# Optimization experiments

Measured on AMD Instinct MI355X. Metric: run time of the kernel, lower is better.

## Reference

```python
import jax, jax.numpy as jnp
import numpy as np

W = 5; WW = 25; STEP = 8; DF = 128; NH = 8; DH = 16; EPS = 1e-5


def sinusoid_pe(ww, d):
    pos = np.arange(ww)[:, None].astype(np.float32)
    div = np.exp(np.arange(0, d, 2).astype(np.float32) * (-np.log(10000.0) / d))
    pe = np.zeros((ww, d), np.float32)
    pe[:, 0::2] = np.sin(pos * div)
    pe[:, 1::2] = np.cos(pos * div)
    return jnp.asarray(pe)


def ln(x, s, b):
    m = x.mean(-1, keepdims=True)
    v = ((x - m) ** 2).mean(-1, keepdims=True)
    return (x - m) / jnp.sqrt(v + EPS) * s + b


def attn_layer(x, src, wq, wk, wv, wm, m1w, m1b, m2w, m2b, n1s, n1b, n2s, n2b):
    N, T, D = x.shape
    q = (x @ wq).reshape(N, T, NH, DH)
    k = (src @ wk).reshape(N, T, NH, DH)
    v = (src @ wv).reshape(N, T, NH, DH)
    a = jax.nn.softmax(jnp.einsum('nqhd,nkhd->nhqk', q, k) * (DH ** -0.5), axis=-1)
    msg = jnp.einsum('nhqk,nkhd->nqhd', a, v).reshape(N, T, D) @ wm
    msg = ln(msg, n1s, n1b)
    h = jnp.concatenate([x, msg], axis=-1)
    h = jax.nn.relu(h @ m1w + m1b) @ m2w + m2b
    return x + ln(h, n2s, n2b)


def local_transformer(x0, x1, P):
    names = ['self', 'cross', 'self', 'cross']
    for i, nm in enumerate(names):
        p = tuple(a[i] for a in P)
        if nm == 'self':
            x0 = attn_layer(x0, x0, *p)
            x1 = attn_layer(x1, x1, *p)
        else:
            x0 = attn_layer(x0, x1, *p)
            x1 = attn_layer(x1, x0, *p)
    return x0, x1


def unfold_window(fm):
    # F.unfold(kernel=5, stride=4, pad=2) then 'B (C MM) L -> B L MM C'
    B, C, H, Wd = fm.shape
    pat = jax.lax.conv_general_dilated_patches(fm, (W, W), (4, 4), [(W // 2, W // 2)] * 2)
    Ho, Wo = pat.shape[2], pat.shape[3]
    pat = pat.reshape(B, C, WW, Ho * Wo)  # channel-major ordering matches torch unfold
    return pat.transpose(0, 3, 2, 1)  # [B, L, WW, C]


def forward(mdesc0, mdesc1, fine0, fine1, conv_w, conv_b, proj_w, proj_b,
            merge_w, merge_b, reg1_w, reg1_b, reg2_w, reg2_b, reg_w, reg_b,
            lt_wq, lt_wk, lt_wv, lt_wm, lt_m1w, lt_m1b, lt_m2w, lt_m2b,
            lt_n1s, lt_n1b, lt_n2s, lt_n2b):
    B, L, Dc = mdesc0.shape
    Wc = int(np.sqrt(L))
    # dual-softmax confidence matrix
    sim = jnp.einsum('bld,bmd->blm', mdesc0 / Dc, mdesc1 / Dc) / 0.1
    cm = jax.nn.softmax(sim, axis=1) * jax.nn.softmax(sim, axis=2)
    # mutual nearest-neighbor filter (static-shape: keep all B*L rows + mask)
    mut = (cm == cm.max(axis=2, keepdims=True)) & (cm == cm.max(axis=1, keepdims=True))
    cf = cm * mut
    mask = cf.max(axis=2) > 0  # [B, L]
    j = jnp.argmax(cf, axis=2)  # [B, L]
    # 1x1 conv to fine dim
    f0 = jnp.einsum('bchw,oc->bohw', fine0, conv_w[:, :, 0, 0]) + conv_b[None, :, None, None]
    f1 = jnp.einsum('bchw,oc->bohw', fine1, conv_w[:, :, 0, 0]) + conv_b[None, :, None, None]
    u0 = unfold_window(f0)
    u1 = unfold_window(f1)  # [B, L, WW, DF]
    N = B * L
    b_all = jnp.repeat(jnp.arange(B), L)
    idx1 = b_all * L + j.reshape(-1)
    local0 = u0.reshape(N, WW, DF)
    local1 = u1.reshape(N, WW, DF)[idx1]
    c0 = mdesc0.reshape(N, Dc)
    c1 = mdesc1.reshape(N, Dc)[idx1]
    local = jnp.concatenate([local0, local1], axis=0)  # [2N, WW, DF]
    center = jnp.concatenate([c0, c1], axis=0) @ proj_w + proj_b  # [2N, DF]
    center = jnp.broadcast_to(center[:, None, :], (2 * N, WW, DF))
    ld = jnp.concatenate([local, center], axis=-1) @ merge_w + merge_b
    ld = ld + sinusoid_pe(WW, DF)[None]
    d0, d1 = ld[:N], ld[N:]
    P = (lt_wq, lt_wk, lt_wv, lt_wm, lt_m1w, lt_m1b, lt_m2w, lt_m2b, lt_n1s, lt_n1b, lt_n2s, lt_n2b)
    fd0, fd1 = local_transformer(d0, d1, P)
    c = WW // 2
    cen = jnp.broadcast_to(fd0[:, c:c + 1, :], (N, WW, DF))
    feat = jnp.concatenate([cen, fd1], axis=-1)  # [N, WW, 2*DF]
    feat = feat @ reg1_w + reg1_b  # [N, WW, DF]
    feat = feat.reshape(N, WW * DF)  # [N, 3200]
    feat = feat @ reg2_w + reg2_b  # dropout is identity at eval
    coords = feat @ reg_w + reg_b  # [N, 2]
    xj = (j % Wc) * STEP
    yj = (j // Wc) * STEP
    base = jnp.stack([xj, yj], axis=-1).reshape(N, 2).astype(coords.dtype)
    return (base + coords) * mask.reshape(N, 1).astype(coords.dtype)


def setup_inputs():
    key = jax.random.key(0)
    ks = jax.random.split(key, 24)
    B, L, Dc = 2, 2304, 256
    Hf = 192
    nl = 4

    def rn(k, shape, fan):
        return jax.random.normal(k, shape, jnp.float32) * (fan ** -0.5)

    return {
        'mdesc0': jax.random.normal(ks[0], (B, L, Dc), jnp.float32),
        'mdesc1': jax.random.normal(ks[1], (B, L, Dc), jnp.float32),
        'fine0': jax.random.normal(ks[2], (B, Dc, Hf, Hf), jnp.float32),
        'fine1': jax.random.normal(ks[3], (B, Dc, Hf, Hf), jnp.float32),
        'conv_w': rn(ks[4], (DF, Dc, 1, 1), Dc),
        'conv_b': jnp.zeros((DF,), jnp.float32),
        'proj_w': rn(ks[5], (Dc, DF), Dc),
        'proj_b': jnp.zeros((DF,), jnp.float32),
        'merge_w': rn(ks[6], (2 * DF, DF), 2 * DF),
        'merge_b': jnp.zeros((DF,), jnp.float32),
        'reg1_w': rn(ks[7], (2 * DF, DF), 2 * DF),
        'reg1_b': jnp.zeros((DF,), jnp.float32),
        'reg2_w': rn(ks[8], (WW * DF, DF), WW * DF),
        'reg2_b': jnp.zeros((DF,), jnp.float32),
        'reg_w': rn(ks[9], (DF, 2), DF),
        'reg_b': jnp.zeros((2,), jnp.float32),
        'lt_wq': rn(ks[10], (nl, DF, DF), DF),
        'lt_wk': rn(ks[11], (nl, DF, DF), DF),
        'lt_wv': rn(ks[12], (nl, DF, DF), DF),
        'lt_wm': rn(ks[13], (nl, DF, DF), DF),
        'lt_m1w': rn(ks[14], (nl, 2 * DF, 2 * DF), 2 * DF),
        'lt_m1b': jnp.zeros((nl, 2 * DF), jnp.float32),
        'lt_m2w': rn(ks[15], (nl, 2 * DF, DF), 2 * DF),
        'lt_m2b': jnp.zeros((nl, DF), jnp.float32),
        'lt_n1s': jnp.ones((nl, DF), jnp.float32),
        'lt_n1b': jnp.zeros((nl, DF), jnp.float32),
        'lt_n2s': jnp.ones((nl, DF), jnp.float32),
        'lt_n2b': jnp.zeros((nl, DF), jnp.float32),
    }


def reference(mdesc0, mdesc1, fine0, fine1, conv_w, conv_b, proj_w, proj_b,
              merge_w, merge_b, reg1_w, reg1_b, reg2_w, reg2_b, reg_w, reg_b,
              lt_wq, lt_wk, lt_wv, lt_wm, lt_m1w, lt_m1b, lt_m2w, lt_m2b,
              lt_n1s, lt_n1b, lt_n2s, lt_n2b):
    return forward(mdesc0, mdesc1, fine0, fine1, conv_w, conv_b, proj_w, proj_b,
                   merge_w, merge_b, reg1_w, reg1_b, reg2_w, reg2_b, reg_w, reg_b,
                   lt_wq, lt_wk, lt_wv, lt_wm, lt_m1w, lt_m1b, lt_m2w, lt_m2b,
                   lt_n1s, lt_n1b, lt_n2s, lt_n2b)
```

## Files before the change

kernel.cpp:

```cpp
#include <hip/hip_runtime.h>
#include <stdint.h>
#include <type_traits>

#define DEVFN static __device__ __forceinline__

typedef __attribute__((ext_vector_type(8))) short bf16x8v;
typedef __attribute__((ext_vector_type(4))) float f32x4v;
typedef __attribute__((ext_vector_type(2))) _Float16 h2;

DEVFN float b2f(short s) {
  union { unsigned u; float f; } c; c.u = ((unsigned)(unsigned short)s) << 16; return c.f;
}
DEVFN short f2b(float f) {
  union { float f; unsigned u; } c; c.f = f;
  unsigned r = c.u + 0x7fffu + ((c.u >> 16) & 1u);
  return (short)(r >> 16);
}
DEVFN short f2h(float f) {
  union { _Float16 h; short s; } c; c.h = (_Float16)f; return c.s;
}
DEVFN void gl_lds16(const void* g, void* l) {
  __builtin_amdgcn_global_load_lds((const __attribute__((address_space(1))) void*)g,
                                   (__attribute__((address_space(3))) void*)l, 16, 0, 0);
}
DEVFN double exp_small(double x) {
  return 1.0 + x * (1.0 + x * (0.5 + x * ((1.0 / 6.0) + x * (1.0 / 24.0))));
}


__global__ void prep_all(const float* __restrict__ conv_w, const float* __restrict__ proj_w,
                         const float* __restrict__ merge_w, const float* __restrict__ reg1_w,
                         const float* __restrict__ reg2_w, const float* __restrict__ wq,
                         const float* __restrict__ wk, const float* __restrict__ wv,
                         const float* __restrict__ wm, const float* __restrict__ m1w,
                         const float* __restrict__ m2w,
                         short* __restrict__ convT, short* __restrict__ projT,
                         short* __restrict__ mergeAT, short* __restrict__ mergeBT,
                         short* __restrict__ reg1T, short* __restrict__ reg2T,
                         short* __restrict__ wqkvT, short* __restrict__ wmT,
                         short* __restrict__ m1T, short* __restrict__ m2T,
                         float* __restrict__ pe, short* __restrict__ zp) {
  const int L0 = 32768, L1 = 32768, L2 = 16384, L3 = 16384, L4 = 32768, L5 = 409600;
  const int L6 = 196608, L7 = 65536, L8 = 262144, L9 = 131072, L10 = 3200, L11 = 128;
  const int TOT = L0+L1+L2+L3+L4+L5+L6+L7+L8+L9+L10+L11;
  for (int gi = blockIdx.x * blockDim.x + threadIdx.x; gi < TOT; gi += gridDim.x * blockDim.x) {
    int i = gi;
    if (i < L0) { convT[i] = f2b(conv_w[i]); continue; } i -= L0;
    if (i < L1) { int n = i >> 8, k = i & 255; projT[i] = f2b(proj_w[k * 128 + n]); continue; } i -= L1;
    if (i < L2) { int n = i >> 7, k = i & 127; mergeAT[i] = f2b(merge_w[k * 128 + n]); continue; } i -= L2;
    if (i < L3) { int n = i >> 7, k = i & 127; mergeBT[i] = f2b(merge_w[(128 + k) * 128 + n]); continue; } i -= L3;
    if (i < L4) { int n = i >> 8, k = i & 255; reg1T[i] = f2b(reg1_w[k * 128 + n]); continue; } i -= L4;
    if (i < L5) { int n = i / 3200, k = i - n * 3200; reg2T[i] = f2b(reg2_w[k * 128 + n]); continue; } i -= L5;
    if (i < L6) {
      int l = i / 49152; int r = i - l * 49152; int w = r / 16384; int r2 = r - w * 16384;
      int n = r2 >> 7, k = r2 & 127;
      const float* s = (w == 0) ? wq : (w == 1) ? wk : wv;
      wqkvT[i] = f2b(s[l * 16384 + k * 128 + n]); continue;
    } i -= L6;
    if (i < L7) { int l = i >> 14; int r = i & 16383; int n = r >> 7, k = r & 127;
      wmT[i] = f2b(wm[l * 16384 + k * 128 + n]); continue; } i -= L7;
    if (i < L8) { int l = i >> 16; int r = i & 65535; int n = r >> 8, k = r & 255;
      m1T[i] = f2b(m1w[l * 65536 + k * 256 + n]); continue; } i -= L8;
    if (i < L9) { int l = i >> 15; int r = i & 32767; int n = r >> 8, k = r & 255;
      m2T[i] = f2b(m2w[l * 32768 + k * 128 + n]); continue; } i -= L9;
    if (i < L10) {
      int t = i >> 7, d = i & 127; int i2 = d >> 1;
      float div = expf(((float)(2 * i2)) * (-logf(10000.f) / 128.f));
      float ang = (float)t * div;
      pe[i] = (d & 1) ? cosf(ang) : sinf(ang); continue;
    } i -= L10;
    zp[i] = 0;
  }
}


__global__ __launch_bounds__(256) void sim_gemm(const float* __restrict__ A,
                                                const float* __restrict__ Bm,
                                                float* __restrict__ S) {
  int b = blockIdx.z;
  A += (size_t)b * 2304 * 256; Bm += (size_t)b * 2304 * 256; S += (size_t)b * 2304 * 2304;
  __shared__ float As[96][33], Bs[96][33];
  int tid = threadIdx.x;
  int tx = tid & 15, ty = tid >> 4;
  int rb = blockIdx.x * 96, cb = blockIdx.y * 96;
  float acc[6][6] = {};
  for (int k0 = 0; k0 < 256; k0 += 32) {
    #pragma unroll
    for (int s = 0; s < 3; ++s) {
      int slot = s * 256 + tid;
      int r = slot >> 3, cq = slot & 7;
      float4 va = *(const float4*)&A[(size_t)(rb + r) * 256 + k0 + 4 * cq];
      float4 vb = *(const float4*)&Bm[(size_t)(cb + r) * 256 + k0 + 4 * cq];
      As[r][4 * cq] = va.x; As[r][4 * cq + 1] = va.y; As[r][4 * cq + 2] = va.z; As[r][4 * cq + 3] = va.w;
      Bs[r][4 * cq] = vb.x; Bs[r][4 * cq + 1] = vb.y; Bs[r][4 * cq + 2] = vb.z; Bs[r][4 * cq + 3] = vb.w;
    }
    __syncthreads();
    #pragma unroll 4
    for (int k = 0; k < 32; ++k) {
      float av[6], bv[6];
      #pragma unroll
      for (int i = 0; i < 6; ++i) av[i] = As[ty + 16 * i][k];
      #pragma unroll
      for (int j = 0; j < 6; ++j) bv[j] = Bs[tx + 16 * j][k];
      #pragma unroll
      for (int i = 0; i < 6; ++i)
        #pragma unroll
        for (int j = 0; j < 6; ++j) acc[i][j] += av[i] * bv[j];
    }
    __syncthreads();
  }
  #pragma unroll
  for (int i = 0; i < 6; ++i)
    #pragma unroll
    for (int j = 0; j < 6; ++j) {
      float t = acc[i][j] * (1.0f / 65536.0f);
      S[(size_t)(rb + ty + 16 * i) * 2304 + cb + tx + 16 * j] = t / 0.1f;
    }
}

__global__ __launch_bounds__(256) void row_lse(const float* __restrict__ S, double* __restrict__ lnR) {
  int row = blockIdx.x;
  const float* Sp = S + (size_t)row * 2304;
  double a = 0;
  for (int m = threadIdx.x; m < 2304; m += 256) a += exp_small((double)Sp[m]);
  __shared__ double red[256];
  red[threadIdx.x] = a; __syncthreads();
  for (int s = 128; s > 0; s >>= 1) { if (threadIdx.x < (unsigned)s) red[threadIdx.x] += red[threadIdx.x + s]; __syncthreads(); }
  if (!threadIdx.x) lnR[row] = log(red[0]);
}

__global__ __launch_bounds__(256) void col_part(const float* __restrict__ S,
                                                const double* __restrict__ lnR,
                                                double* __restrict__ psum,
                                                double* __restrict__ pkey,
                                                int* __restrict__ pidx) {
  int bb = blockIdx.z;
  int c0 = blockIdx.x * 64;
  int rc = blockIdx.y;
  int col = c0 + (threadIdx.x & 63);
  int g = threadIdx.x >> 6;
  const float* Sp = S + (size_t)bb * 2304 * 2304;
  const double* lr = lnR + bb * 2304;
  double a = 0, best = -1e300; int bi = 1 << 30;
  int l0 = rc * 192;
  for (int t = g; t < 192; t += 4) {
    int l = l0 + t;
    double sv = (double)Sp[(size_t)l * 2304 + col];
    a += exp_small(sv);
    double k = 2.0 * sv - lr[l];
    if (k > best || (k == best && l < bi)) { best = k; bi = l; }
  }
  __shared__ double s_sum[256]; __shared__ double s_key[256]; __shared__ int s_idx[256];
  s_sum[threadIdx.x] = a; s_key[threadIdx.x] = best; s_idx[threadIdx.x] = bi;
  __syncthreads();
  if (g == 0) {
    double ts = a; double tk = best; int ti = bi;
    #pragma unroll
    for (int gg = 1; gg < 4; ++gg) {
      int o = threadIdx.x + gg * 64;
      ts += s_sum[o];
      if (s_key[o] > tk || (s_key[o] == tk && s_idx[o] < ti)) { tk = s_key[o]; ti = s_idx[o]; }
    }
    size_t off = ((size_t)bb * 12 + rc) * 2304 + col;
    psum[off] = ts; pkey[off] = tk; pidx[off] = ti;
  }
}

__global__ void col_reduce(const double* __restrict__ psum, const double* __restrict__ pkey,
                           const int* __restrict__ pidx, double* __restrict__ lnC,
                           int* __restrict__ CB) {
  int i = blockIdx.x * blockDim.x + threadIdx.x;
  if (i >= 4608) return;
  int bb = i / 2304, col = i - bb * 2304;
  double s = 0; double bk = -1e300; int bi = 1 << 30;
  for (int rc = 0; rc < 12; ++rc) {
    size_t off = ((size_t)bb * 12 + rc) * 2304 + col;
    s += psum[off];
    double k = pkey[off]; int ix = pidx[off];
    if (k > bk || (k == bk && ix < bi)) { bk = k; bi = ix; }
  }
  lnC[i] = log(s);
  CB[i] = bi;
}

__global__ __launch_bounds__(256) void row_argmax(const float* __restrict__ S,
                                                  const double* __restrict__ lnC,
                                                  int* __restrict__ J) {
  int row = blockIdx.x; int bb = row / 2304;
  const float* Sp = S + (size_t)row * 2304;
  const double* lc = lnC + bb * 2304;
  double best = -1e300; int bi = 1 << 30;
  for (int m = threadIdx.x; m < 2304; m += 256) {
    double k = 2.0 * (double)Sp[m] - lc[m];
    if (k > best || (k == best && m < bi)) { best = k; bi = m; }
  }
  __shared__ double bvs[256]; __shared__ int bis[256];
  bvs[threadIdx.x] = best; bis[threadIdx.x] = bi; __syncthreads();
  for (int s = 128; s > 0; s >>= 1) {
    if (threadIdx.x < (unsigned)s) {
      double ov = bvs[threadIdx.x + s]; int oi = bis[threadIdx.x + s];
      if (ov > bvs[threadIdx.x] || (ov == bvs[threadIdx.x] && oi < bis[threadIdx.x])) { bvs[threadIdx.x] = ov; bis[threadIdx.x] = oi; }
    }
    __syncthreads();
  }
  if (!threadIdx.x) J[row] = bis[0];
}


__global__ __launch_bounds__(256) void transpose_fine(const float* __restrict__ src, short* __restrict__ dst) {
  __shared__ float t[64][65];
  int bb = blockIdx.z, p0 = blockIdx.x * 64, c0 = blockIdx.y * 64;
  for (int i = threadIdx.x; i < 1024; i += 256) {
    int cl = i >> 4, pl = (i & 15) * 4;
    float4 v = *(const float4*)&src[((size_t)(bb * 256 + c0 + cl)) * 36864 + p0 + pl];
    t[cl][pl] = v.x; t[cl][pl + 1] = v.y; t[cl][pl + 2] = v.z; t[cl][pl + 3] = v.w;
  }
  __syncthreads();
  for (int i = threadIdx.x; i < 1024; i += 256) {
    int pl = i >> 4, cg = (i & 15) * 4;
    unsigned w0 = (unsigned short)f2b(t[cg][pl]) | ((unsigned)(unsigned short)f2b(t[cg + 1][pl]) << 16);
    unsigned w1 = (unsigned short)f2b(t[cg + 2][pl]) | ((unsigned)(unsigned short)f2b(t[cg + 3][pl]) << 16);
    int2 v; v.x = (int)w0; v.y = (int)w1;
    *(int2*)&dst[((size_t)(bb * 36864 + p0 + pl)) * 256 + c0 + cg] = v;
  }
}

__global__ void cgather(const float* __restrict__ md0, const float* __restrict__ md1,
                        const int* __restrict__ J, short* __restrict__ cbuf) {
  int total = 9216 * 256;
  for (int i = blockIdx.x * blockDim.x + threadIdx.x; i < total; i += gridDim.x * blockDim.x) {
    int w = i >> 8, c = i & 255;
    const float* src;
    if (w < 4608) src = md0 + (size_t)w * 256;
    else {
      int n = w - 4608; int bb = n / 2304;
      src = md1 + (size_t)(bb * 2304 + J[n]) * 256;
    }
    cbuf[i] = f2b(src[c]);
  }
}

__global__ void build_tab(const int* __restrict__ J, const short* __restrict__ f0c,
                          const short* __restrict__ f1c, const short* __restrict__ zp,
                          unsigned long long* __restrict__ tab) {
  int total = 230400;
  for (int i = blockIdx.x * blockDim.x + threadIdx.x; i < total; i += gridDim.x * blockDim.x) {
    int w = i / 25, t = i - w * 25;
    int bb, cell; const short* fc;
    if (w < 4608) { bb = w / 2304; cell = w - bb * 2304; fc = f0c; }
    else { int n = w - 4608; bb = n / 2304; cell = J[n]; fc = f1c; }
    int cy = cell / 48, cx = cell - cy * 48;
    int y = cy * 4 - 2 + t / 5, x = cx * 4 - 2 + t % 5;
    const short* p = (y >= 0 && y < 192 && x >= 0 && x < 192)
                   ? fc + (size_t)((bb * 192 + y) * 192 + x) * 128 : zp;
    tab[i] = (unsigned long long)(uintptr_t)p;
  }
}


constexpr int AM_LIN = 0, AM_DUAL = 1, AM_TAB = 2, AM_CEN = 3;
constexpr int EP_BIAS = 0, EP_BF32 = 1, EP_RELU = 2, EP_LN = 3, EP_LNRES = 4, EP_MERGE = 5, EP_PART = 6, EP_F16 = 7;

template<int AMODE, int EPI>
__global__ __launch_bounds__(256)
void gemm_bf16(const short* __restrict__ A1, const short* __restrict__ A2,
               const unsigned long long* __restrict__ tab,
               const short* __restrict__ Wt, int M, int Kd, int kstr, int K1,
               const float* __restrict__ bias, int bstride,
               const float* __restrict__ lns, const float* __restrict__ lnb,
               const short* __restrict__ resid,
               const float* __restrict__ ccp, const float* __restrict__ pep,
               short* __restrict__ outb, float* __restrict__ outf, int ldc,
               long wstride, long ostride) {
  __shared__ __align__(16) short As[128 * 64];
  __shared__ __align__(16) short Bs[128 * 64];
  __shared__ float rsum[2][128], rsq[2][128];
  int tid = threadIdx.x, lane = tid & 63, wid = tid >> 6;
  int wr = wid >> 1, wc = wid & 1;
  int nwg = gridDim.x;
  int orig = blockIdx.x;
  int qd = nwg >> 3, rm = nwg & 7;
  int xcd = orig & 7, offx = orig >> 3;
  int bx = (xcd < rm ? xcd * (qd + 1) : rm * (qd + 1) + (xcd - rm) * qd) + offx;
  int rb = bx * 128;
  int by = blockIdx.y;
  int koff = blockIdx.z * Kd;
  const short* Wsel = Wt + (size_t)by * wstride;
  const float* bsel = bias ? bias + (size_t)by * bstride : nullptr;
  short* osel_b = outb ? outb + (size_t)by * ostride : nullptr;
  float* osel_f = outf ? outf + (size_t)by * ostride : nullptr;

  f32x4v acc[4][4];
  #pragma unroll
  for (int i = 0; i < 4; ++i)
    #pragma unroll
    for (int j = 0; j < 4; ++j) acc[i][j] = (f32x4v){0.f, 0.f, 0.f, 0.f};

  for (int k0 = 0; k0 < Kd; k0 += 64) {
    #pragma unroll
    for (int q = 0; q < 4; ++q) {
      int i = (wid * 4 + q) * 64 + lane;
      int r = i >> 3, pch = i & 7;
      int c = pch ^ (r & 7);
      const short* src;
      if (AMODE == AM_LIN) {
        src = A1 + (size_t)(rb + r) * kstr + koff + k0 + c * 8;
      } else if (AMODE == AM_DUAL) {
        if (k0 < K1) src = A1 + (size_t)(rb + r) * K1 + k0 + c * 8;
        else         src = A2 + (size_t)(rb + r) * (Kd - K1) + (k0 - K1) + c * 8;
      } else if (AMODE == AM_CEN) {
        int rg = rb + r;
        if (k0 < K1) src = A1 + (size_t)((rg / 25) * 25 + 12) * K1 + k0 + c * 8;
        else         src = A2 + (size_t)rg * (Kd - K1) + (k0 - K1) + c * 8;
      } else {
        src = (const short*)(uintptr_t)tab[rb + r] + k0 + c * 8;
      }
      gl_lds16(src, &As[(size_t)i * 8]);
    }
    #pragma unroll
    for (int q = 0; q < 4; ++q) {
      int i = (wid * 4 + q) * 64 + lane;
      int r = i >> 3, pch = i & 7;
      int c = pch ^ (r & 7);
      gl_lds16(Wsel + (size_t)r * kstr + koff + k0 + c * 8, &Bs[(size_t)i * 8]);
    }
    __syncthreads();
    #pragma unroll
    for (int kk = 0; kk < 2; ++kk) {
      bf16x8v af[4], bfr[4];
      #pragma unroll
      for (int mi = 0; mi < 4; ++mi) {
        int r = wr * 64 + mi * 16 + (lane & 15);
        int c = kk * 4 + (lane >> 4);
        int pch = c ^ (r & 7);
        af[mi] = *(const bf16x8v*)&As[r * 64 + pch * 8];
      }
      #pragma unroll
      for (int ni = 0; ni < 4; ++ni) {
        int r = wc * 64 + ni * 16 + (lane & 15);
        int c = kk * 4 + (lane >> 4);
        int pch = c ^ (r & 7);
        bfr[ni] = *(const bf16x8v*)&Bs[r * 64 + pch * 8];
      }
      #pragma unroll
      for (int mi = 0; mi < 4; ++mi)
        #pragma unroll
        for (int ni = 0; ni < 4; ++ni)
          acc[mi][ni] = __builtin_amdgcn_mfma_f32_16x16x32_bf16(af[mi], bfr[ni], acc[mi][ni], 0, 0, 0);
    }
    __syncthreads();
  }

  int colloc[4];
  #pragma unroll
  for (int ni = 0; ni < 4; ++ni) colloc[ni] = wc * 64 + ni * 16 + (lane & 15);
  float bv[4];
  #pragma unroll
  for (int ni = 0; ni < 4; ++ni)
    bv[ni] = (EPI == EP_MERGE || EPI == EP_PART) ? 0.f : (bsel ? bsel[colloc[ni]] : 0.f);

  #pragma unroll
  for (int mi = 0; mi < 4; ++mi)
    #pragma unroll
    for (int ni = 0; ni < 4; ++ni)
      #pragma unroll
      for (int q = 0; q < 4; ++q) {
        float v = acc[mi][ni][q] + bv[ni];
        if (EPI == EP_RELU) v = fmaxf(v, 0.f);
        acc[mi][ni][q] = v;
      }

  if (EPI == EP_LN || EPI == EP_LNRES) {
    #pragma unroll
    for (int mi = 0; mi < 4; ++mi)
      #pragma unroll
      for (int q = 0; q < 4; ++q) {
        float s = 0.f, ss = 0.f;
        #pragma unroll
        for (int ni = 0; ni < 4; ++ni) { float v = acc[mi][ni][q]; s += v; ss += v * v; }
        s += __shfl_xor(s, 1, 64); ss += __shfl_xor(ss, 1, 64);
        s += __shfl_xor(s, 2, 64); ss += __shfl_xor(ss, 2, 64);
        s += __shfl_xor(s, 4, 64); ss += __shfl_xor(ss, 4, 64);
        s += __shfl_xor(s, 8, 64); ss += __shfl_xor(ss, 8, 64);
        int rl = wr * 64 + mi * 16 + (lane >> 4) * 4 + q;
        if ((lane & 15) == 0) { rsum[wc][rl] = s; rsq[wc][rl] = ss; }
      }
    __syncthreads();
  }

  #pragma unroll
  for (int mi = 0; mi < 4; ++mi)
    #pragma unroll
    for (int q = 0; q < 4; ++q) {
      int rl = wr * 64 + mi * 16 + (lane >> 4) * 4 + q;
      long rg = rb + rl;
      float mean = 0.f, rstd = 0.f;
      if (EPI == EP_LN || EPI == EP_LNRES) {
        float s = rsum[0][rl] + rsum[1][rl];
        float ss = rsq[0][rl] + rsq[1][rl];
        mean = s * (1.f / 128.f);
        float var = ss * (1.f / 128.f) - mean * mean;
        rstd = 1.f / sqrtf(var + 1e-5f);
      }
      int wv_ = 0, tv_ = 0;
      if (EPI == EP_MERGE) { wv_ = (int)(rg / 25); tv_ = (int)(rg - (long)wv_ * 25); }
      #pragma unroll
      for (int ni = 0; ni < 4; ++ni) {
        int cg = colloc[ni];
        float v = acc[mi][ni][q];
        if (EPI == EP_MERGE) v += ccp[(size_t)wv_ * 128 + cg] + pep[tv_ * 128 + cg];
        if (EPI == EP_LN || EPI == EP_LNRES) {
          v = (v - mean) * rstd * lns[cg] + lnb[cg];
          if (EPI == EP_LNRES) v += b2f(resid[(size_t)rg * 128 + cg]);
        }
        if (EPI == EP_BF32) osel_f[(size_t)rg * ldc + cg] = v;
        else if (EPI == EP_PART) osel_f[((size_t)blockIdx.z * M + rg) * ldc + cg] = v;
        else if (EPI == EP_F16) osel_b[(size_t)rg * ldc + cg] = f2h(v);
        else osel_b[(size_t)rg * ldc + cg] = f2b(v);
      }
    }
}

__global__ void reduce_part(const float* __restrict__ part, const float* __restrict__ bias,
                            short* __restrict__ out) {
  int i = blockIdx.x * blockDim.x + threadIdx.x;
  if (i >= 4608 * 128) return;
  int c = i & 127;
  float s = bias[c];
  #pragma unroll
  for (int z = 0; z < 5; ++z) s += part[(size_t)z * 4608 * 128 + i];
  out[i] = f2b(s);
}


template<bool CROSS>
__global__ __launch_bounds__(256)
void qkv_fused(const short* __restrict__ xq, const short* __restrict__ xkv,
               const short* __restrict__ wqkv, short* __restrict__ out, long ostride) {
  __shared__ __align__(16) short As[128 * 128];
  __shared__ __align__(16) short Bs[128 * 64];
  int tid = threadIdx.x, lane = tid & 63, wid = tid >> 6;
  int wr = wid >> 1, wc = wid & 1;
  int nwg = gridDim.x;
  int orig = blockIdx.x;
  int qd = nwg >> 3, rm = nwg & 7;
  int xcd = orig & 7, offx = orig >> 3;
  int bx = (xcd < rm ? xcd * (qd + 1) : rm * (qd + 1) + (xcd - rm) * qd) + offx;
  int rb = bx * 128;

  auto stageA = [&](const short* src) {
    #pragma unroll
    for (int q = 0; q < 8; ++q) {
      int i = (wid * 8 + q) * 64 + lane;
      int r = i >> 4, pch = i & 15;
      int c = pch ^ (r & 7);
      gl_lds16(src + (size_t)(rb + r) * 128 + c * 8, &As[(size_t)i * 8]);
    }
  };
  stageA(xq);

  #pragma unroll
  for (int w = 0; w < 3; ++w) {
    if (CROSS && w == 1) stageA(xkv);
    f32x4v acc[4][4];
    #pragma unroll
    for (int i = 0; i < 4; ++i)
      #pragma unroll
      for (int j = 0; j < 4; ++j) acc[i][j] = (f32x4v){0.f, 0.f, 0.f, 0.f};
    const short* Wsel = wqkv + (size_t)w * 16384;

    #pragma unroll
    for (int kt = 0; kt < 2; ++kt) {
      int k0 = kt * 64;
      #pragma unroll
      for (int q = 0; q < 4; ++q) {
        int i = (wid * 4 + q) * 64 + lane;
        int r = i >> 3, pch = i & 7;
        int c = pch ^ (r & 7);
        gl_lds16(Wsel + (size_t)r * 128 + k0 + c * 8, &Bs[(size_t)i * 8]);
      }
      __syncthreads();
      #pragma unroll
      for (int kk = 0; kk < 2; ++kk) {
        bf16x8v af[4], bfr[4];
        #pragma unroll
        for (int mi = 0; mi < 4; ++mi) {
          int r = wr * 64 + mi * 16 + (lane & 15);
          int cg = kt * 8 + kk * 4 + (lane >> 4);
          int pch = cg ^ (r & 7);
          af[mi] = *(const bf16x8v*)&As[r * 128 + pch * 8];
        }
        #pragma unroll
        for (int ni = 0; ni < 4; ++ni) {
          int r = wc * 64 + ni * 16 + (lane & 15);
          int c = kk * 4 + (lane >> 4);
          int pch = c ^ (r & 7);
          bfr[ni] = *(const bf16x8v*)&Bs[r * 64 + pch * 8];
        }
        #pragma unroll
        for (int mi = 0; mi < 4; ++mi)
          #pragma unroll
          for (int ni = 0; ni < 4; ++ni)
            acc[mi][ni] = __builtin_amdgcn_mfma_f32_16x16x32_bf16(af[mi], bfr[ni], acc[mi][ni], 0, 0, 0);
      }
      __syncthreads();
    }
    short* ow = out + (size_t)w * ostride;
    #pragma unroll
    for (int mi = 0; mi < 4; ++mi)
      #pragma unroll
      for (int q = 0; q < 4; ++q) {
        int rl = wr * 64 + mi * 16 + (lane >> 4) * 4 + q;
        long rg = rb + rl;
        #pragma unroll
        for (int ni = 0; ni < 4; ++ni) {
          int cg = wc * 64 + ni * 16 + (lane & 15);
          ow[(size_t)rg * 128 + cg] = f2h(acc[mi][ni][q]);
        }
      }
  }
}


__global__ __launch_bounds__(256)
void mlp2_fused(const short* __restrict__ x, const short* __restrict__ attnout,
                const short* __restrict__ wmT,
                const short* __restrict__ m1wT, const short* __restrict__ m2wT,
                const float* __restrict__ n1s, const float* __restrict__ n1b,
                const float* __restrict__ b1, const float* __restrict__ b2,
                const float* __restrict__ lns, const float* __restrict__ lnb,
                short* __restrict__ out) {
  __shared__ __align__(16) short AsHs[64 * 128];
  __shared__ __align__(16) short Bs[128 * 128];
  __shared__ __align__(16) short Ms[64 * 128];
  short* As = AsHs;
  short* Hs = AsHs;
  float* rsum = (float*)AsHs;
  float* rsq  = (float*)AsHs + 128;
  int tid = threadIdx.x, lane = tid & 63, wid = tid >> 6;
  int wr = wid >> 1, wc = wid & 1;
  int nwg = gridDim.x;
  int orig = blockIdx.x;
  int qd = nwg >> 3, rm = nwg & 7;
  int xcd = orig & 7, offx = orig >> 3;
  int bx = (xcd < rm ? xcd * (qd + 1) : rm * (qd + 1) + (xcd - rm) * qd) + offx;
  int rb = bx * 64;

  int colloc[4];
  #pragma unroll
  for (int ni = 0; ni < 4; ++ni) colloc[ni] = wc * 64 + ni * 16 + (lane & 15);

  auto stageA = [&](const short* src) {
    #pragma unroll
    for (int q = 0; q < 4; ++q) {
      int i = (wid * 4 + q) * 64 + lane;
      int r = i >> 4, pch = i & 15;
      int c = pch ^ (r & 7);
      gl_lds16(src + (size_t)(rb + r) * 128 + c * 8, &As[(size_t)i * 8]);
    }
  };
  auto stageB = [&](const short* src, int kstr) {
    #pragma unroll
    for (int q = 0; q < 8; ++q) {
      int i = (wid * 8 + q) * 64 + lane;
      int r = i >> 4, pch = i & 15;
      int c = pch ^ (r & 7);
      gl_lds16(src + (size_t)r * kstr + c * 8, &Bs[(size_t)i * 8]);
    }
  };
  auto mfmaAB = [&](const short* Atile, f32x4v (*acc)[4]) {
    #pragma unroll
    for (int kk = 0; kk < 4; ++kk) {
      bf16x8v af[2], bfr[4];
      #pragma unroll
      for (int mi = 0; mi < 2; ++mi) {
        int r = wr * 32 + mi * 16 + (lane & 15);
        int c = kk * 4 + (lane >> 4);
        int pch = c ^ (r & 7);
        af[mi] = *(const bf16x8v*)&Atile[r * 128 + pch * 8];
      }
      #pragma unroll
      for (int ni = 0; ni < 4; ++ni) {
        int r = wc * 64 + ni * 16 + (lane & 15);
        int c = kk * 4 + (lane >> 4);
        int pch = c ^ (r & 7);
        bfr[ni] = *(const bf16x8v*)&Bs[r * 128 + pch * 8];
      }
      #pragma unroll
      for (int mi = 0; mi < 2; ++mi)
        #pragma unroll
        for (int ni = 0; ni < 4; ++ni)
          acc[mi][ni] = __builtin_amdgcn_mfma_f32_16x16x32_bf16(af[mi], bfr[ni], acc[mi][ni], 0, 0, 0);
    }
  };

  {
    f32x4v acc0[2][4];
    #pragma unroll
    for (int i = 0; i < 2; ++i)
      #pragma unroll
      for (int j = 0; j < 4; ++j) acc0[i][j] = (f32x4v){0.f, 0.f, 0.f, 0.f};
    stageA(attnout);
    stageB(wmT, 128);
    __syncthreads();
    mfmaAB(As, acc0);
    __syncthreads();
    #pragma unroll
    for (int mi = 0; mi < 2; ++mi)
      #pragma unroll
      for (int q = 0; q < 4; ++q) {
        float s = 0.f, ss = 0.f;
        #pragma unroll
        for (int ni = 0; ni < 4; ++ni) { float v = acc0[mi][ni][q]; s += v; ss += v * v; }
        s += __shfl_xor(s, 1, 64); ss += __shfl_xor(ss, 1, 64);
        s += __shfl_xor(s, 2, 64); ss += __shfl_xor(ss, 2, 64);
        s += __shfl_xor(s, 4, 64); ss += __shfl_xor(ss, 4, 64);
        s += __shfl_xor(s, 8, 64); ss += __shfl_xor(ss, 8, 64);
        int rl = wr * 32 + mi * 16 + (lane >> 4) * 4 + q;
        if ((lane & 15) == 0) { rsum[wc * 64 + rl] = s; rsq[wc * 64 + rl] = ss; }
      }
    __syncthreads();
    #pragma unroll
    for (int mi = 0; mi < 2; ++mi)
      #pragma unroll
      for (int q = 0; q < 4; ++q) {
        int rl = wr * 32 + mi * 16 + (lane >> 4) * 4 + q;
        float s = rsum[rl] + rsum[64 + rl];
        float ss = rsq[rl] + rsq[64 + rl];
        float mean = s * (1.f / 128.f);
        float var = ss * (1.f / 128.f) - mean * mean;
        float rstd = 1.f / sqrtf(var + 1e-5f);
        #pragma unroll
        for (int ni = 0; ni < 4; ++ni) {
          int cg = colloc[ni];
          float v = (acc0[mi][ni][q] - mean) * rstd * n1s[cg] + n1b[cg];
          int c = cg >> 3, pch = c ^ (rl & 7);
          Ms[rl * 128 + pch * 8 + (cg & 7)] = f2b(v);
        }
      }
    __syncthreads();
  }

  f32x4v acc2[2][4];
  #pragma unroll
  for (int i = 0; i < 2; ++i)
    #pragma unroll
    for (int j = 0; j < 4; ++j) acc2[i][j] = (f32x4v){0.f, 0.f, 0.f, 0.f};

  #pragma unroll
  for (int nh = 0; nh < 2; ++nh) {
    f32x4v acc1[2][4];
    #pragma unroll
    for (int i = 0; i < 2; ++i)
      #pragma unroll
      for (int j = 0; j < 4; ++j) acc1[i][j] = (f32x4v){0.f, 0.f, 0.f, 0.f};

    stageA(x);
    stageB(m1wT + (size_t)(nh * 128) * 256, 256);
    __syncthreads();
    mfmaAB(As, acc1);
    __syncthreads();
    stageB(m1wT + (size_t)(nh * 128) * 256 + 128, 256);
    __syncthreads();
    mfmaAB(Ms, acc1);
    __syncthreads();
    #pragma unroll
    for (int mi = 0; mi < 2; ++mi)
      #pragma unroll
      for (int q = 0; q < 4; ++q) {
        int rl = wr * 32 + mi * 16 + (lane >> 4) * 4 + q;
        #pragma unroll
        for (int ni = 0; ni < 4; ++ni) {
          int cg = wc * 64 + ni * 16 + (lane & 15);
          float v = fmaxf(acc1[mi][ni][q] + b1[nh * 128 + cg], 0.f);
          int c = cg >> 3, pch = c ^ (rl & 7);
          Hs[rl * 128 + pch * 8 + (cg & 7)] = f2b(v);
        }
      }
    __syncthreads();
    stageB(m2wT + nh * 128, 256);
    __syncthreads();
    mfmaAB(Hs, acc2);
    __syncthreads();
  }

  #pragma unroll
  for (int mi = 0; mi < 2; ++mi)
    #pragma unroll
    for (int ni = 0; ni < 4; ++ni)
      #pragma unroll
      for (int q = 0; q < 4; ++q)
        acc2[mi][ni][q] += b2[colloc[ni]];

  #pragma unroll
  for (int mi = 0; mi < 2; ++mi)
    #pragma unroll
    for (int q = 0; q < 4; ++q) {
      float s = 0.f, ss = 0.f;
      #pragma unroll
      for (int ni = 0; ni < 4; ++ni) { float v = acc2[mi][ni][q]; s += v; ss += v * v; }
      s += __shfl_xor(s, 1, 64); ss += __shfl_xor(ss, 1, 64);
      s += __shfl_xor(s, 2, 64); ss += __shfl_xor(ss, 2, 64);
      s += __shfl_xor(s, 4, 64); ss += __shfl_xor(ss, 4, 64);
      s += __shfl_xor(s, 8, 64); ss += __shfl_xor(ss, 8, 64);
      int rl = wr * 32 + mi * 16 + (lane >> 4) * 4 + q;
      if ((lane & 15) == 0) { rsum[wc * 64 + rl] = s; rsq[wc * 64 + rl] = ss; }
    }
  __syncthreads();

  #pragma unroll
  for (int mi = 0; mi < 2; ++mi)
    #pragma unroll
    for (int q = 0; q < 4; ++q) {
      int rl = wr * 32 + mi * 16 + (lane >> 4) * 4 + q;
      long rg = rb + rl;
      float s = rsum[rl] + rsum[64 + rl];
      float ss = rsq[rl] + rsq[64 + rl];
      float mean = s * (1.f / 128.f);
      float var = ss * (1.f / 128.f) - mean * mean;
      float rstd = 1.f / sqrtf(var + 1e-5f);
      #pragma unroll
      for (int ni = 0; ni < 4; ++ni) {
        int cg = colloc[ni];
        float v = (acc2[mi][ni][q] - mean) * rstd * lns[cg] + lnb[cg];
        v += b2f(x[(size_t)rg * 128 + cg]);
        out[(size_t)rg * 128 + cg] = f2b(v);
      }
    }
}


__global__ __launch_bounds__(256) void attn_win(const short* __restrict__ Q,
                                                const short* __restrict__ K,
                                                const short* __restrict__ V,
                                                short* __restrict__ Mo) {
  int w = blockIdx.x;
  const short* Qg = Q + (size_t)w * 3200;
  const short* Kg = K + (size_t)w * 3200;
  const short* Vg = V + (size_t)w * 3200;
  __shared__ short Qs[25 * 136 + 8], Ks[25 * 136 + 8], Vs[25 * 136 + 8];
  int tid = threadIdx.x;
  for (int s = tid; s < 400; s += 256) {
    int r = s >> 4, ch = s & 15;
    *(int4*)&Qs[r * 136 + ch * 8] = ((const int4*)Qg)[s];
    *(int4*)&Ks[r * 136 + ch * 8] = ((const int4*)Kg)[s];
    *(int4*)&Vs[r * 136 + ch * 8] = ((const int4*)Vg)[s];
  }
  __syncthreads();

  int wid = tid >> 6, lane = tid & 63;
  int half = lane >> 5, li = lane & 31;
  int h = wid * 2 + half;
  if (li < 25) {
    int i = li;
    h2 qr[8];
    #pragma unroll
    for (int t = 0; t < 8; ++t) qr[t] = *(const h2*)&Qs[i * 136 + h * 16 + t * 2];
    float p[25];
    float mx = -1e30f;
    #pragma unroll
    for (int jx = 0; jx < 25; ++jx) {
      const short* kr = &Ks[jx * 136 + h * 16];
      float s = 0.f;
      #pragma unroll
      for (int t = 0; t < 8; ++t)
        s = __builtin_amdgcn_fdot2(qr[t], *(const h2*)&kr[t * 2], s, false);
      s *= 0.25f;
      p[jx] = s;
      mx = fmaxf(mx, s);
    }
    float sum = 0.f;
    #pragma unroll
    for (int jx = 0; jx < 25; ++jx) { float e = expf(p[jx] - mx); p[jx] = e; sum += e; }
    float inv = 1.f / sum;
    h2 o2[8];
    #pragma unroll
    for (int t = 0; t < 8; ++t) { o2[t][0] = (_Float16)0.f; o2[t][1] = (_Float16)0.f; }
    #pragma unroll
    for (int jx = 0; jx < 25; ++jx) {
      _Float16 ph = (_Float16)(p[jx] * inv);
      h2 pv; pv[0] = ph; pv[1] = ph;
      const short* vr = &Vs[jx * 136 + h * 16];
      #pragma unroll
      for (int t = 0; t < 8; ++t) o2[t] += pv * (*(const h2*)&vr[t * 2]);
    }
    int* outp = (int*)(Mo + (size_t)w * 3200 + i * 128 + h * 16);
    #pragma unroll
    for (int t = 0; t < 8; ++t) {
      unsigned lo = (unsigned short)f2b((float)o2[t][0]);
      unsigned hi = (unsigned short)f2b((float)o2[t][1]);
      outp[t] = (int)(lo | (hi << 16));
    }
  }
}


__global__ void final_reg(const short* __restrict__ fv, const float* __restrict__ regw,
                          const float* __restrict__ regb, const int* __restrict__ J,
                          const int* __restrict__ CB, float* __restrict__ out) {
  int n = blockIdx.x * blockDim.x + threadIdx.x;
  if (n >= 4608) return;
  const short* f = fv + (size_t)n * 128;
  float c0 = regb[0], c1 = regb[1];
  for (int d = 0; d < 128; ++d) { float v = b2f(f[d]); c0 += v * regw[d * 2]; c1 += v * regw[d * 2 + 1]; }
  int jv = J[n]; int bb = n / 2304;
  int msk = (CB[bb * 2304 + jv] == (n - bb * 2304)) ? 1 : 0;
  float bx = (float)((jv % 48) * 8), by = (float)((jv / 48) * 8);
  out[n * 2] = msk ? (bx + c0) : 0.f;
  out[n * 2 + 1] = msk ? (by + c1) : 0.f;
}


extern "C" void kernel_launch(void* const* d_in, const int* in_sizes, int n_in,
                              void* d_out, int out_size, void* d_ws, size_t ws_size,
                              hipStream_t stream) {
  const float* md0 = (const float*)d_in[0];
  const float* md1 = (const float*)d_in[1];
  const float* fine0 = (const float*)d_in[2];
  const float* fine1 = (const float*)d_in[3];
  const float* conv_w = (const float*)d_in[4];
  const float* conv_b = (const float*)d_in[5];
  const float* proj_w = (const float*)d_in[6];
  const float* proj_b = (const float*)d_in[7];
  const float* merge_w = (const float*)d_in[8];
  const float* merge_b = (const float*)d_in[9];
  const float* reg1_w = (const float*)d_in[10];
  const float* reg1_b = (const float*)d_in[11];
  const float* reg2_w = (const float*)d_in[12];
  const float* reg2_b = (const float*)d_in[13];
  const float* reg_w = (const float*)d_in[14];
  const float* reg_b = (const float*)d_in[15];
  const float* wq_f = (const float*)d_in[16];
  const float* wk_f = (const float*)d_in[17];
  const float* wv_f = (const float*)d_in[18];
  const float* wm_f = (const float*)d_in[19];
  const float* m1w = (const float*)d_in[20];
  const float* m1b = (const float*)d_in[21];
  const float* m2w = (const float*)d_in[22];
  const float* m2b = (const float*)d_in[23];
  const float* n1s = (const float*)d_in[24];
  const float* n1b = (const float*)d_in[25];
  const float* n2s = (const float*)d_in[26];
  const float* n2b = (const float*)d_in[27];

  char* ws = (char*)d_ws;
  const size_t SZX = (size_t)230400 * 128 * 2;
  const size_t TAILSZ = 20 * 1024 * 1024;
  int CHM = 57600;
  if (SZX + 3ull * 230400 * 256 + TAILSZ <= ws_size)      CHM = 230400;
  else if (SZX + 3ull * 115200 * 256 + TAILSZ <= ws_size) CHM = 115200;
  const size_t CHR = (size_t)CHM * 256;

  short* X  = (short*)(ws);
  char*  Rb = ws + SZX;
  short* R0 = (short*)(Rb);
  short* R1 = (short*)(Rb + CHR);
  short* R2 = (short*)(Rb + 2 * CHR);
  float* S    = (float*)Rb;
  short* F0C  = (short*)Rb;
  short* F1C  = (short*)(Rb + (size_t)73728 * 128 * 2);
  short* FT   = X;
  short* FB   = (short*)Rb;
  float* PART = (float*)(Rb + 2 * CHR);

  char* p = ws + SZX + 3 * CHR;
  double* lnR = (double*)p; p += 4608 * 8;
  double* lnC = (double*)p; p += 4608 * 8;
  int* J = (int*)p; p += 4608 * 4;
  int* CBst = (int*)p; p += 4608 * 4;
  double* PSUM = (double*)p; p += (size_t)2 * 12 * 2304 * 8;
  double* PKEY = (double*)p; p += (size_t)2 * 12 * 2304 * 8;
  int* PIDX = (int*)p; p += (size_t)2 * 12 * 2304 * 4;
  short* CBUF = (short*)p; p += (size_t)9216 * 256 * 2;
  short* CEN = (short*)p; p += (size_t)9216 * 128 * 2;
  float* CC = (float*)p; p += (size_t)9216 * 128 * 4;
  unsigned long long* TAB = (unsigned long long*)p; p += (size_t)230400 * 8;
  float* PE = (float*)p; p += 3200 * 4;
  short* ZP = (short*)p; p += 256;
  short* convT = (short*)p; p += 128 * 256 * 2;
  short* projT = (short*)p; p += 128 * 256 * 2;
  short* mergeAT = (short*)p; p += 128 * 128 * 2;
  short* mergeBT = (short*)p; p += 128 * 128 * 2;
  short* reg1T = (short*)p; p += 128 * 256 * 2;
  short* reg2T = (short*)p; p += (size_t)128 * 3200 * 2;
  short* wqkvT = (short*)p; p += (size_t)4 * 3 * 128 * 128 * 2;
  short* wmT = (short*)p; p += 4 * 128 * 128 * 2;
  short* m1T = (short*)p; p += 4 * 256 * 256 * 2;
  short* m2T = (short*)p; p += (size_t)4 * 128 * 256 * 2;
  short* FV = (short*)p; p += (size_t)4608 * 128 * 2;

  const int TQ = 115200;

  prep_all<<<512, 256, 0, stream>>>(conv_w, proj_w, merge_w, reg1_w, reg2_w,
                                    wq_f, wk_f, wv_f, wm_f, m1w, m2w,
                                    convT, projT, mergeAT, mergeBT, reg1T, reg2T,
                                    wqkvT, wmT, m1T, m2T, PE, ZP);

  sim_gemm<<<dim3(24, 24, 2), 256, 0, stream>>>(md0, md1, S);
  row_lse<<<4608, 256, 0, stream>>>(S, lnR);
  col_part<<<dim3(36, 12, 2), 256, 0, stream>>>(S, lnR, PSUM, PKEY, PIDX);
  col_reduce<<<18, 256, 0, stream>>>(PSUM, PKEY, PIDX, lnC, CBst);
  row_argmax<<<4608, 256, 0, stream>>>(S, lnC, J);

  auto gemm = [&](auto amode, auto epi, const short* A1, const short* A2,
                  const unsigned long long* tab, const short* Wt, int M, int Kd, int kstr, int K1,
                  const float* bias, int bstride, const float* lns, const float* lnb,
                  const short* resid, const float* cc, const float* pe,
                  short* outb, float* outf, int ldc, int NB, int NZ, long wstride, long ostride) {
    constexpr int AM = decltype(amode)::value, EP = decltype(epi)::value;
    gemm_bf16<AM, EP><<<dim3(M / 128, NB, NZ), 256, 0, stream>>>(
        A1, A2, tab, Wt, M, Kd, kstr, K1, bias, bstride, lns, lnb, resid, cc, pe,
        outb, outf, ldc, wstride, ostride);
  };
  using I0 = std::integral_constant<int, 0>; using I1 = std::integral_constant<int, 1>;
  using I2 = std::integral_constant<int, 2>; using I3 = std::integral_constant<int, 3>;
  using E0 = std::integral_constant<int, 0>; using E1 = std::integral_constant<int, 1>;
  using E5 = std::integral_constant<int, 5>; using E6 = std::integral_constant<int, 6>;

  transpose_fine<<<dim3(576, 4, 2), 256, 0, stream>>>(fine0, FT);
  gemm(I0{}, E0{}, FT, nullptr, nullptr, convT, 73728, 256, 256, 0, conv_b, 0, nullptr, nullptr, nullptr, nullptr, nullptr, F0C, nullptr, 128, 1, 1, 0, 0);
  transpose_fine<<<dim3(576, 4, 2), 256, 0, stream>>>(fine1, FT);
  gemm(I0{}, E0{}, FT, nullptr, nullptr, convT, 73728, 256, 256, 0, conv_b, 0, nullptr, nullptr, nullptr, nullptr, nullptr, F1C, nullptr, 128, 1, 1, 0, 0);

  cgather<<<4608, 256, 0, stream>>>(md0, md1, J, CBUF);
  gemm(I0{}, E0{}, CBUF, nullptr, nullptr, projT, 9216, 256, 256, 0, proj_b, 0, nullptr, nullptr, nullptr, nullptr, nullptr, CEN, nullptr, 128, 1, 1, 0, 0);
  gemm(I0{}, E1{}, CEN, nullptr, nullptr, mergeBT, 9216, 128, 128, 0, merge_b, 0, nullptr, nullptr, nullptr, nullptr, nullptr, nullptr, CC, 128, 1, 1, 0, 0);
  build_tab<<<900, 256, 0, stream>>>(J, F0C, F1C, ZP, TAB);
  gemm(I2{}, E5{}, nullptr, nullptr, TAB, mergeAT, 230400, 128, 128, 0, nullptr, 0, nullptr, nullptr, nullptr, CC, PE, X, nullptr, 128, 1, 1, 0, 0);

  auto pass = [&](int i, const short* xq, const short* xkv, short* xout, int Mtotal, bool cross) {
    const short* wqkv = wqkvT + (size_t)i * 3 * 16384;
    const short* wm = wmT + i * 16384;
    const short* m1 = m1T + i * 65536;
    const short* m2 = m2T + i * 32768;
    for (int off = 0; off < Mtotal; off += CHM) {
      int Mc = (Mtotal - off < CHM) ? (Mtotal - off) : CHM;
      const short* xqc = xq + (size_t)off * 128;
      const short* xkvc = xkv + (size_t)off * 128;
      if (cross)
        qkv_fused<true><<<Mc / 128, 256, 0, stream>>>(xqc, xkvc, wqkv, R0, (long)CHM * 128);
      else
        qkv_fused<false><<<Mc / 128, 256, 0, stream>>>(xqc, xkvc, wqkv, R0, (long)CHM * 128);
      attn_win<<<Mc / 25, 256, 0, stream>>>(R0, R1, R2, R0);
      mlp2_fused<<<Mc / 64, 256, 0, stream>>>(xqc, R0, wm, m1, m2,
                                              n1s + i * 128, n1b + i * 128,
                                              m1b + i * 256, m2b + i * 128,
                                              n2s + i * 128, n2b + i * 128,
                                              xout + (size_t)off * 128);
    }
  };
  short* X1 = X + (size_t)TQ * 128;
  for (int i = 0; i < 4; ++i) {
    if ((i & 1) == 0) {
      pass(i, X, X, X, 230400, false);
    } else {
      pass(i, X, X1, X, TQ, true);
      pass(i, X1, X, X1, TQ, true);
    }
  }

  gemm(I3{}, E0{}, X, X1, nullptr, reg1T, TQ, 256, 256, 128, reg1_b, 0, nullptr, nullptr, nullptr, nullptr, nullptr, FB, nullptr, 128, 1, 1, 0, 0);
  gemm(I0{}, E6{}, FB, nullptr, nullptr, reg2T, 4608, 640, 3200, 0, nullptr, 0, nullptr, nullptr, nullptr, nullptr, nullptr, nullptr, PART, 128, 1, 5, 0, 0);
  reduce_part<<<2304, 256, 0, stream>>>(PART, reg2_b, FV);
  final_reg<<<18, 256, 0, stream>>>(FV, reg_w, reg_b, J, CBst, (float*)d_out);
}
```

Before: 1.495 ms.

## Halve LDS footprint in fused MLP kernel via 64-wide K staging

```diff
diff --git a/kernel.cpp b/kernel.cpp
--- a/kernel.cpp
+++ b/kernel.cpp
@@ -453,7 +453,7 @@
     for (int q = 0; q < 8; ++q) {
       int i = (wid * 8 + q) * 64 + lane;
       int r = i >> 4, pch = i & 15;
-      int c = pch ^ (r & 7);
+      int c = pch ^ (r & 15);
       gl_lds16(src + (size_t)(rb + r) * 128 + c * 8, &As[(size_t)i * 8]);
     }
   };
@@ -487,7 +487,7 @@
         for (int mi = 0; mi < 4; ++mi) {
           int r = wr * 64 + mi * 16 + (lane & 15);
           int cg = kt * 8 + kk * 4 + (lane >> 4);
-          int pch = cg ^ (r & 7);
+          int pch = cg ^ (r & 15);
           af[mi] = *(const bf16x8v*)&As[r * 128 + pch * 8];
         }
         #pragma unroll
@@ -530,13 +530,11 @@
                 const float* __restrict__ b1, const float* __restrict__ b2,
                 const float* __restrict__ lns, const float* __restrict__ lnb,
                 short* __restrict__ out) {
-  __shared__ __align__(16) short AsHs[64 * 128];
-  __shared__ __align__(16) short Bs[128 * 128];
+  __shared__ __align__(16) short AsH[64 * 64];
+  __shared__ __align__(16) short Bs[128 * 64];
   __shared__ __align__(16) short Ms[64 * 128];
-  short* As = AsHs;
-  short* Hs = AsHs;
-  float* rsum = (float*)AsHs;
-  float* rsq  = (float*)AsHs + 128;
+  float* rsum = (float*)AsH;
+  float* rsq  = (float*)AsH + 128;
   int tid = threadIdx.x, lane = tid & 63, wid = tid >> 6;
   int wr = wid >> 1, wc = wid & 1;
   int nwg = gridDim.x;
@@ -550,41 +548,41 @@
   #pragma unroll
   for (int ni = 0; ni < 4; ++ni) colloc[ni] = wc * 64 + ni * 16 + (lane & 15);
 
-  auto stageA = [&](const short* src) {
+  auto stageAh = [&](const short* src, int k0) {
+    #pragma unroll
+    for (int q = 0; q < 2; ++q) {
+      int i = (wid * 2 + q) * 64 + lane;
+      int r = i >> 3, pch = i & 7;
+      int c = pch ^ (r & 7);
+      gl_lds16(src + (size_t)(rb + r) * 128 + k0 + c * 8, &AsH[(size_t)i * 8]);
+    }
+  };
+  auto stageBh = [&](const short* src, int kstr) {
     #pragma unroll
     for (int q = 0; q < 4; ++q) {
       int i = (wid * 4 + q) * 64 + lane;
-      int r = i >> 4, pch = i & 15;
-      int c = pch ^ (r & 7);
-      gl_lds16(src + (size_t)(rb + r) * 128 + c * 8, &As[(size_t)i * 8]);
-    }
-  };
-  auto stageB = [&](const short* src, int kstr) {
-    #pragma unroll
-    for (int q = 0; q < 8; ++q) {
-      int i = (wid * 8 + q) * 64 + lane;
-      int r = i >> 4, pch = i & 15;
+      int r = i >> 3, pch = i & 7;
       int c = pch ^ (r & 7);
       gl_lds16(src + (size_t)r * kstr + c * 8, &Bs[(size_t)i * 8]);
     }
   };
-  auto mfmaAB = [&](const short* Atile, f32x4v (*acc)[4]) {
-    #pragma unroll
-    for (int kk = 0; kk < 4; ++kk) {
+  auto mfmaA = [&](f32x4v (*acc)[4]) {
+    #pragma unroll
+    for (int kk = 0; kk < 2; ++kk) {
       bf16x8v af[2], bfr[4];
       #pragma unroll
       for (int mi = 0; mi < 2; ++mi) {
         int r = wr * 32 + mi * 16 + (lane & 15);
         int c = kk * 4 + (lane >> 4);
         int pch = c ^ (r & 7);
-        af[mi] = *(const bf16x8v*)&Atile[r * 128 + pch * 8];
+        af[mi] = *(const bf16x8v*)&AsH[r * 64 + pch * 8];
       }
       #pragma unroll
       for (int ni = 0; ni < 4; ++ni) {
         int r = wc * 64 + ni * 16 + (lane & 15);
         int c = kk * 4 + (lane >> 4);
         int pch = c ^ (r & 7);
-        bfr[ni] = *(const bf16x8v*)&Bs[r * 128 + pch * 8];
+        bfr[ni] = *(const bf16x8v*)&Bs[r * 64 + pch * 8];
       }
       #pragma unroll
       for (int mi = 0; mi < 2; ++mi)
@@ -593,25 +591,39 @@
           acc[mi][ni] = __builtin_amdgcn_mfma_f32_16x16x32_bf16(af[mi], bfr[ni], acc[mi][ni], 0, 0, 0);
     }
   };
-
-  {
-    f32x4v acc0[2][4];
-    #pragma unroll
-    for (int i = 0; i < 2; ++i)
-      #pragma unroll
-      for (int j = 0; j < 4; ++j) acc0[i][j] = (f32x4v){0.f, 0.f, 0.f, 0.f};
-    stageA(attnout);
-    stageB(wmT, 128);
-    __syncthreads();
-    mfmaAB(As, acc0);
-    __syncthreads();
+  auto mfmaM = [&](int mh, f32x4v (*acc)[4]) {
+    #pragma unroll
+    for (int kk = 0; kk < 2; ++kk) {
+      bf16x8v af[2], bfr[4];
+      #pragma unroll
+      for (int mi = 0; mi < 2; ++mi) {
+        int r = wr * 32 + mi * 16 + (lane & 15);
+        int cg = mh * 8 + kk * 4 + (lane >> 4);
+        int pch = cg ^ (r & 15);
+        af[mi] = *(const bf16x8v*)&Ms[r * 128 + pch * 8];
+      }
+      #pragma unroll
+      for (int ni = 0; ni < 4; ++ni) {
+        int r = wc * 64 + ni * 16 + (lane & 15);
+        int c = kk * 4 + (lane >> 4);
+        int pch = c ^ (r & 7);
+        bfr[ni] = *(const bf16x8v*)&Bs[r * 64 + pch * 8];
+      }
+      #pragma unroll
+      for (int mi = 0; mi < 2; ++mi)
+        #pragma unroll
+        for (int ni = 0; ni < 4; ++ni)
+          acc[mi][ni] = __builtin_amdgcn_mfma_f32_16x16x32_bf16(af[mi], bfr[ni], acc[mi][ni], 0, 0, 0);
+    }
+  };
+  auto lnstats = [&](f32x4v (*acc)[4]) {
     #pragma unroll
     for (int mi = 0; mi < 2; ++mi)
       #pragma unroll
       for (int q = 0; q < 4; ++q) {
         float s = 0.f, ss = 0.f;
         #pragma unroll
-        for (int ni = 0; ni < 4; ++ni) { float v = acc0[mi][ni][q]; s += v; ss += v * v; }
+        for (int ni = 0; ni < 4; ++ni) { float v = acc[mi][ni][q]; s += v; ss += v * v; }
         s += __shfl_xor(s, 1, 64); ss += __shfl_xor(ss, 1, 64);
         s += __shfl_xor(s, 2, 64); ss += __shfl_xor(ss, 2, 64);
         s += __shfl_xor(s, 4, 64); ss += __shfl_xor(ss, 4, 64);
@@ -619,6 +631,42 @@
         int rl = wr * 32 + mi * 16 + (lane >> 4) * 4 + q;
         if ((lane & 15) == 0) { rsum[wc * 64 + rl] = s; rsq[wc * 64 + rl] = ss; }
       }
+  };
+  auto writeHh = [&](int hh, int nh, f32x4v (*acc)[4]) {
+    if (wc == hh) {
+      #pragma unroll
+      for (int mi = 0; mi < 2; ++mi)
+        #pragma unroll
+        for (int q = 0; q < 4; ++q) {
+          int rl = wr * 32 + mi * 16 + (lane >> 4) * 4 + q;
+          #pragma unroll
+          for (int ni = 0; ni < 4; ++ni) {
+            int cl = ni * 16 + (lane & 15);
+            float v = fmaxf(acc[mi][ni][q] + b1[nh * 128 + hh * 64 + cl], 0.f);
+            int c = cl >> 3, pch = c ^ (rl & 7);
+            AsH[rl * 64 + pch * 8 + (cl & 7)] = f2b(v);
+          }
+        }
+    }
+  };
+
+  {
+    f32x4v acc0[2][4];
+    #pragma unroll
+    for (int i = 0; i < 2; ++i)
+      #pragma unroll
+      for (int j = 0; j < 4; ++j) acc0[i][j] = (f32x4v){0.f, 0.f, 0.f, 0.f};
+    stageAh(attnout, 0);
+    stageBh(wmT, 128);
+    __syncthreads();
+    mfmaA(acc0);
+    __syncthreads();
+    stageAh(attnout, 64);
+    stageBh(wmT + 64, 128);
+    __syncthreads();
+    mfmaA(acc0);
+    __syncthreads();
+    lnstats(acc0);
     __syncthreads();
     #pragma unroll
     for (int mi = 0; mi < 2; ++mi)
@@ -634,7 +682,7 @@
         for (int ni = 0; ni < 4; ++ni) {
           int cg = colloc[ni];
           float v = (acc0[mi][ni][q] - mean) * rstd * n1s[cg] + n1b[cg];
-          int c = cg >> 3, pch = c ^ (rl & 7);
+          int c = cg >> 3, pch = c ^ (rl & 15);
           Ms[rl * 128 + pch * 8 + (cg & 7)] = f2b(v);
         }
       }
@@ -649,38 +697,40 @@
 
   #pragma unroll
   for (int nh = 0; nh < 2; ++nh) {
+    const short* m1b_ = m1wT + (size_t)(nh * 128) * 256;
     f32x4v acc1[2][4];
     #pragma unroll
     for (int i = 0; i < 2; ++i)
       #pragma unroll
       for (int j = 0; j < 4; ++j) acc1[i][j] = (f32x4v){0.f, 0.f, 0.f, 0.f};
 
-    stageA(x);
-    stageB(m1wT + (size_t)(nh * 128) * 256, 256);
-    __syncthreads();
-    mfmaAB(As, acc1);
-    __syncthreads();
-    stageB(m1wT + (size_t)(nh * 128) * 256 + 128, 256);
-    __syncthreads();
-    mfmaAB(Ms, acc1);
-    __syncthreads();
-    #pragma unroll
-    for (int mi = 0; mi < 2; ++mi)
-      #pragma unroll
-      for (int q = 0; q < 4; ++q) {
-        int rl = wr * 32 + mi * 16 + (lane >> 4) * 4 + q;
-        #pragma unroll
-        for (int ni = 0; ni < 4; ++ni) {
-          int cg = wc * 64 + ni * 16 + (lane & 15);
-          float v = fmaxf(acc1[mi][ni][q] + b1[nh * 128 + cg], 0.f);
-          int c = cg >> 3, pch = c ^ (rl & 7);
-          Hs[rl * 128 + pch * 8 + (cg & 7)] = f2b(v);
-        }
-      }
-    __syncthreads();
-    stageB(m2wT + nh * 128, 256);
-    __syncthreads();
-    mfmaAB(Hs, acc2);
+    stageAh(x, 0);
+    stageBh(m1b_, 256);
+    __syncthreads();
+    mfmaA(acc1);
+    __syncthreads();
+    stageAh(x, 64);
+    stageBh(m1b_ + 64, 256);
+    __syncthreads();
+    mfmaA(acc1);
+    __syncthreads();
+    stageBh(m1b_ + 128, 256);
+    __syncthreads();
+    mfmaM(0, acc1);
+    __syncthreads();
+    stageBh(m1b_ + 192, 256);
+    __syncthreads();
+    mfmaM(1, acc1);
+    __syncthreads();
+    writeHh(0, nh, acc1);
+    stageBh(m2wT + nh * 128, 256);
+    __syncthreads();
+    mfmaA(acc2);
+    __syncthreads();
+    writeHh(1, nh, acc1);
+    stageBh(m2wT + nh * 128 + 64, 256);
+    __syncthreads();
+    mfmaA(acc2);
     __syncthreads();
   }
 
@@ -692,20 +742,7 @@
       for (int q = 0; q < 4; ++q)
         acc2[mi][ni][q] += b2[colloc[ni]];
 
-  #pragma unroll
-  for (int mi = 0; mi < 2; ++mi)
-    #pragma unroll
-    for (int q = 0; q < 4; ++q) {
-      float s = 0.f, ss = 0.f;
-      #pragma unroll
-      for (int ni = 0; ni < 4; ++ni) { float v = acc2[mi][ni][q]; s += v; ss += v * v; }
-      s += __shfl_xor(s, 1, 64); ss += __shfl_xor(ss, 1, 64);
-      s += __shfl_xor(s, 2, 64); ss += __shfl_xor(ss, 2, 64);
-      s += __shfl_xor(s, 4, 64); ss += __shfl_xor(ss, 4, 64);
-      s += __shfl_xor(s, 8, 64); ss += __shfl_xor(ss, 8, 64);
-      int rl = wr * 32 + mi * 16 + (lane >> 4) * 4 + q;
-      if ((lane & 15) == 0) { rsum[wc * 64 + rl] = s; rsq[wc * 64 + rl] = ss; }
-    }
+  lnstats(acc2);
   __syncthreads();
 
   #pragma unroll
```

Result: slower. 1.549 ms (+3.6%).
